# Kernel tuning notes

Measured on AMD Instinct MI355X. Metric: run time of the kernel, lower is better.

Reference implementation:

```python
import jax, jax.numpy as jnp
import numpy as np

N = 131072   # octree nodes at this depth
C = 192      # channels (depthwise)
K = 27       # 3x3x3 neighbor stencil
BN_EPS = 1e-5


def setup_inputs() -> dict:
    key = jax.random.key(0)
    k1, k2, k3 = jax.random.split(key, 3)
    data = jax.random.normal(k1, (N, C), dtype=jnp.float32)
    # Octree neighbor table: for each node, indices of its 27 stencil neighbors.
    neigh = jax.random.randint(k2, (N, K), 0, N)
    # Depthwise weights [K, C] (OctreeDWConv, use_bias=False)
    weight = jax.random.normal(k3, (K, C), dtype=jnp.float32) * 0.05
    gamma = jnp.ones((C,), dtype=jnp.float32)
    beta = jnp.zeros((C,), dtype=jnp.float32)
    return {"data": data, "neigh": neigh, "weight": weight,
            "gamma": gamma, "beta": beta}


def reference(data, neigh, weight, gamma, beta):
    # Depthwise octree conv: out[n, c] = sum_k data[neigh[n, k], c] * weight[k, c]
    # Scan over the 27 stencil taps so we never materialize the [N, K, C] gather.
    def step(acc, kin):
        idx_k, w_k = kin          # idx_k: [N], w_k: [C]
        return acc + data[idx_k] * w_k, None

    acc0 = jnp.zeros_like(data)
    out, _ = jax.lax.scan(step, acc0, (neigh.T, weight))  # out: [N, C]

    # BatchNorm1d (training mode: batch statistics over the node dimension)
    mean = jnp.mean(out, axis=0)
    var = jnp.var(out, axis=0)
    return (out - mean) * jax.lax.rsqrt(var + BN_EPS) * gamma + beta
```

## Files before the change

### kernel.cpp

```cpp
#include <hip/hip_runtime.h>


static constexpr int NN = 131072;
static constexpr int CC = 192;
static constexpr int KK = 27;
static constexpr int NB = 32;
static constexpr float BN_EPS = 1e-5f;

typedef float          f32x4 __attribute__((ext_vector_type(4)));
typedef unsigned short u16x4 __attribute__((ext_vector_type(4)));
typedef unsigned int   u32x4 __attribute__((ext_vector_type(4)));

__device__ __forceinline__ unsigned short f2bf_rne(float x) {
    unsigned u = __float_as_uint(x);
    return (unsigned short)((u + 0x7FFFu + ((u >> 16) & 1u)) >> 16);
}
__device__ __forceinline__ float bf2f(unsigned short b) {
    return __uint_as_float((unsigned)b << 16);
}

__global__ __launch_bounds__(256) void cvt_zero(
    const float* __restrict__ src, unsigned short* __restrict__ dst,
    float* __restrict__ stats )
{
    if (blockIdx.x < 2 && threadIdx.x < CC)
        stats[blockIdx.x * CC + threadIdx.x] = 0.f;

    const int tot    = NN * CC / 4;
    const int stride = gridDim.x * 256;
    for (int i = blockIdx.x * 256 + threadIdx.x; i < tot; i += stride) {
        const f32x4 v = __builtin_nontemporal_load(
            reinterpret_cast<const f32x4*>(src) + i);
        u16x4 o;
        o.x = f2bf_rne(v.x); o.y = f2bf_rne(v.y);
        o.z = f2bf_rne(v.z); o.w = f2bf_rne(v.w);
        reinterpret_cast<u16x4*>(dst)[i] = o;
    }
}

__global__ __launch_bounds__(192, 6) void conv_r8(
    const unsigned short* __restrict__ data_bf,
    const int*   __restrict__ neigh,
    const float* __restrict__ weight,
    unsigned short* __restrict__ conv_bf,
    float*       __restrict__ ch_sum,
    float*       __restrict__ ch_sumsq)
{
    const int c    = threadIdx.x;
    const int base = blockIdx.x * NB;

    float w[KK];
#pragma unroll
    for (int k = 0; k < KK; ++k) w[k] = weight[k * CC + c];

    float s = 0.f, ss = 0.f;

    for (int n = 0; n < NB; ++n) {
        const int node = base + n;
        const int* nrow = neigh + (size_t)node * KK;

        unsigned short r[KK];
#pragma unroll
        for (int k = 0; k < KK; ++k)
            r[k] = data_bf[(size_t)nrow[k] * CC + c];

        float acc = 0.f;
#pragma unroll
        for (int k = 0; k < KK; ++k)
            acc = fmaf(bf2f(r[k]), w[k], acc);

        __builtin_nontemporal_store(f2bf_rne(acc),
                                    &conv_bf[(size_t)node * CC + c]);
        s  += acc;
        ss += acc * acc;
    }

    atomicAdd(&ch_sum[c],   s);
    atomicAdd(&ch_sumsq[c], ss);
}

__global__ __launch_bounds__(192) void bn_apply_fused(
    const u32x4* __restrict__ conv_u4,
    const float* __restrict__ ch_sum,
    const float* __restrict__ ch_sumsq,
    const float* __restrict__ gamma,
    const float* __restrict__ beta,
    float* __restrict__ out)
{
    const int t  = threadIdx.x;
    const int cb = (t % 24) * 8;

    const float inv_n = 1.0f / (float)NN;
    float sc[8], bi[8];
#pragma unroll
    for (int j = 0; j < 8; ++j) {
        const float m = ch_sum[cb + j] * inv_n;
        const float v = ch_sumsq[cb + j] * inv_n - m * m;
        sc[j] = gamma[cb + j] * rsqrtf(v + BN_EPS);
        bi[j] = beta[cb + j] - m * sc[j];
    }

    f32x4* __restrict__ out4 = reinterpret_cast<f32x4*>(out);
    for (int nb = blockIdx.x; nb < NN / 8; nb += gridDim.x) {
        const int i8 = nb * 192 + t;
        const u32x4 u = __builtin_nontemporal_load(conv_u4 + i8);
        f32x4 a, b;
        a.x = fmaf(__uint_as_float(u.x << 16),         sc[0], bi[0]);
        a.y = fmaf(__uint_as_float(u.x & 0xFFFF0000u), sc[1], bi[1]);
        a.z = fmaf(__uint_as_float(u.y << 16),         sc[2], bi[2]);
        a.w = fmaf(__uint_as_float(u.y & 0xFFFF0000u), sc[3], bi[3]);
        b.x = fmaf(__uint_as_float(u.z << 16),         sc[4], bi[4]);
        b.y = fmaf(__uint_as_float(u.z & 0xFFFF0000u), sc[5], bi[5]);
        b.z = fmaf(__uint_as_float(u.w << 16),         sc[6], bi[6]);
        b.w = fmaf(__uint_as_float(u.w & 0xFFFF0000u), sc[7], bi[7]);
        __builtin_nontemporal_store(a, out4 + 2 * i8);
        __builtin_nontemporal_store(b, out4 + 2 * i8 + 1);
    }
}

__global__ __launch_bounds__(CC) void conv_bn_partial_f32(
    const float* __restrict__ data,
    const int*   __restrict__ neigh,
    const float* __restrict__ weight,
    float*       __restrict__ conv_out,
    float*       __restrict__ ch_sum,
    float*       __restrict__ ch_sumsq)
{
    const int c = threadIdx.x;
    const int base = blockIdx.x * NB;
    float w[KK];
#pragma unroll
    for (int k = 0; k < KK; ++k) w[k] = weight[k * CC + c];
    float s = 0.f, ss = 0.f;
    for (int n = 0; n < NB; ++n) {
        const int node = base + n;
        const int* nrow = neigh + node * KK;
        float acc = 0.f;
#pragma unroll
        for (int k = 0; k < KK; ++k)
            acc = fmaf(data[nrow[k] * CC + c], w[k], acc);
        conv_out[node * CC + c] = acc;
        s += acc; ss += acc * acc;
    }
    atomicAdd(&ch_sum[c], s);
    atomicAdd(&ch_sumsq[c], ss);
}

__global__ __launch_bounds__(192) void bn_apply_f32_fused(
    float* __restrict__ out,
    const float* __restrict__ ch_sum,
    const float* __restrict__ ch_sumsq,
    const float* __restrict__ gamma,
    const float* __restrict__ beta)
{
    const int t = threadIdx.x;
    const int g = t / 48;
    const int q = t - g * 48;
    const int cb = q * 4;
    const float inv_n = 1.0f / (float)NN;
    float4 sc, bi;
    float m0 = ch_sum[cb+0]*inv_n, m1 = ch_sum[cb+1]*inv_n;
    float m2 = ch_sum[cb+2]*inv_n, m3 = ch_sum[cb+3]*inv_n;
    sc.x = gamma[cb+0]*rsqrtf(ch_sumsq[cb+0]*inv_n - m0*m0 + BN_EPS);
    sc.y = gamma[cb+1]*rsqrtf(ch_sumsq[cb+1]*inv_n - m1*m1 + BN_EPS);
    sc.z = gamma[cb+2]*rsqrtf(ch_sumsq[cb+2]*inv_n - m2*m2 + BN_EPS);
    sc.w = gamma[cb+3]*rsqrtf(ch_sumsq[cb+3]*inv_n - m3*m3 + BN_EPS);
    bi.x = beta[cb+0] - m0*sc.x; bi.y = beta[cb+1] - m1*sc.y;
    bi.z = beta[cb+2] - m2*sc.z; bi.w = beta[cb+3] - m3*sc.w;
    for (int nb = blockIdx.x; nb < NN / 4; nb += gridDim.x) {
        const int i = (nb * 4 + g) * 48 + q;
        float4 v = reinterpret_cast<float4*>(out)[i];
        v.x = fmaf(v.x, sc.x, bi.x); v.y = fmaf(v.y, sc.y, bi.y);
        v.z = fmaf(v.z, sc.z, bi.z); v.w = fmaf(v.w, sc.w, bi.w);
        reinterpret_cast<float4*>(out)[i] = v;
    }
}

extern "C" void kernel_launch(void* const* d_in, const int* in_sizes, int n_in,
                              void* d_out, int out_size, void* d_ws, size_t ws_size,
                              hipStream_t stream) {
    const float* data   = (const float*)d_in[0];
    const int*   neigh  = (const int*)  d_in[1];
    const float* weight = (const float*)d_in[2];
    const float* gamma  = (const float*)d_in[3];
    const float* beta   = (const float*)d_in[4];
    float* out = (float*)d_out;

    float* stats    = (float*)d_ws;
    float* ch_sum   = stats;
    float* ch_sumsq = stats + CC;
    unsigned short* data_bf = (unsigned short*)((char*)d_ws + 4096);
    const size_t stage_bytes = (size_t)NN * CC * sizeof(unsigned short);
    unsigned short* conv_bf =
        (unsigned short*)((char*)d_ws + 4096 + stage_bytes);

    const size_t need_full = 4096 + 2 * stage_bytes;

    if (ws_size >= need_full) {
        cvt_zero<<<4096, 256, 0, stream>>>(data, data_bf, stats);
        conv_r8<<<NN / NB, 192, 0, stream>>>(
            data_bf, neigh, weight, conv_bf, ch_sum, ch_sumsq);
        bn_apply_fused<<<4096, 192, 0, stream>>>(
            (const u32x4*)conv_bf, ch_sum, ch_sumsq, gamma, beta, out);
    } else {
        hipMemsetAsync(stats, 0, 2 * CC * sizeof(float), stream);
        conv_bn_partial_f32<<<NN / NB, CC, 0, stream>>>(
            data, neigh, weight, out, ch_sum, ch_sumsq);
        bn_apply_f32_fused<<<8192, 192, 0, stream>>>(
            out, ch_sum, ch_sumsq, gamma, beta);
    }
}
```

Measured before the change: 412.6 us.

## Fuse convert, conv, and BN into one cooperative persistent kernel with grid syncs

Replaces the three kernel launches with a single cooperative kernel of 2048 blocks. It converts the input to bf16, runs the gather convolution over two node tiles per block, writes per-block partial statistics into the output buffer, reduces them, and applies BN, with grid.sync between phases. This removes launch gaps and per-block atomics on the stats but adds grid-wide barriers and caps residency at the cooperative grid size. Nontemporal loads and stores are also dropped in the fallback kernels. The old launches remain as a fallback if the cooperative launch fails.

```diff
diff --git a/kernel.cpp b/kernel.cpp
--- a/kernel.cpp
+++ b/kernel.cpp
@@ -1,10 +1,15 @@
 #include <hip/hip_runtime.h>
-
-
-static constexpr int NN = 131072;
-static constexpr int CC = 192;
-static constexpr int KK = 27;
-static constexpr int NB = 32;
+#include <hip/hip_cooperative_groups.h>
+
+namespace cg = cooperative_groups;
+
+
+static constexpr int NN   = 131072;
+static constexpr int CC   = 192;
+static constexpr int KK   = 27;
+static constexpr int NB   = 32;
+static constexpr int GRID = 2048;
+static constexpr int TPB  = 192;
 static constexpr float BN_EPS = 1e-5f;
 
 typedef float          f32x4 __attribute__((ext_vector_type(4)));
@@ -19,18 +24,127 @@
     return __uint_as_float((unsigned)b << 16);
 }
 
+__global__ __launch_bounds__(TPB, 6) void fused_all(
+    const float* __restrict__ data,
+    const int*   __restrict__ neigh,
+    const float* __restrict__ weight,
+    const float* __restrict__ gamma,
+    const float* __restrict__ beta,
+    float*       __restrict__ out,
+    unsigned short* __restrict__ data_bf,
+    unsigned short* __restrict__ conv_bf,
+    float*       __restrict__ stats)
+{
+    cg::grid_group grid = cg::this_grid();
+    const int t   = threadIdx.x;
+    const int bid = blockIdx.x;
+    float* partials = out;
+
+    if (bid < 2) stats[bid * TPB + t] = 0.f;
+    {
+        const int tot    = NN * CC / 4;
+        const int stride = GRID * TPB;
+        for (int i = bid * TPB + t; i < tot; i += stride) {
+            const f32x4 v = reinterpret_cast<const f32x4*>(data)[i];
+            u16x4 o;
+            o.x = f2bf_rne(v.x); o.y = f2bf_rne(v.y);
+            o.z = f2bf_rne(v.z); o.w = f2bf_rne(v.w);
+            reinterpret_cast<u16x4*>(data_bf)[i] = o;
+        }
+    }
+    __threadfence();
+    grid.sync();
+
+    {
+        float w[KK];
+#pragma unroll
+        for (int k = 0; k < KK; ++k) w[k] = weight[k * CC + t];
+
+        float s = 0.f, ss = 0.f;
+#pragma unroll 1
+        for (int gidx = 0; gidx < 2; ++gidx) {
+            const int base = (bid + gidx * GRID) * NB;
+            for (int n = 0; n < NB; ++n) {
+                const int node = base + n;
+                const int* nrow = neigh + (size_t)node * KK;
+
+                unsigned short r[KK];
+#pragma unroll
+                for (int k = 0; k < KK; ++k)
+                    r[k] = data_bf[(size_t)nrow[k] * CC + t];
+
+                float acc = 0.f;
+#pragma unroll
+                for (int k = 0; k < KK; ++k)
+                    acc = fmaf(bf2f(r[k]), w[k], acc);
+
+                conv_bf[(size_t)node * CC + t] = f2bf_rne(acc);
+                s  += acc;
+                ss += acc * acc;
+            }
+        }
+        partials[bid * 384 + t]       = s;
+        partials[bid * 384 + 192 + t] = ss;
+    }
+    __threadfence();
+    grid.sync();
+
+    if (bid < 16) {
+        float a0 = 0.f, a1 = 0.f;
+        const int r0 = bid * (GRID / 16);
+        for (int r = r0; r < r0 + GRID / 16; ++r) {
+            a0 += partials[r * 384 + t];
+            a1 += partials[r * 384 + 192 + t];
+        }
+        atomicAdd(&stats[t],       a0);
+        atomicAdd(&stats[192 + t], a1);
+    }
+    __threadfence();
+    grid.sync();
+
+    {
+        const int cb = (t % 24) * 8;
+        const float inv_n = 1.0f / (float)NN;
+        float sc[8], bi[8];
+#pragma unroll
+        for (int j = 0; j < 8; ++j) {
+            const float m = stats[cb + j] * inv_n;
+            const float v = stats[192 + cb + j] * inv_n - m * m;
+            sc[j] = gamma[cb + j] * rsqrtf(v + BN_EPS);
+            bi[j] = beta[cb + j] - m * sc[j];
+        }
+
+        const u32x4* __restrict__ conv_u4 =
+            reinterpret_cast<const u32x4*>(conv_bf);
+        f32x4* __restrict__ out4 = reinterpret_cast<f32x4*>(out);
+        for (int nb = bid; nb < NN / 8; nb += GRID) {
+            const int i8 = nb * TPB + t;
+            const u32x4 u = conv_u4[i8];
+            f32x4 a, b;
+            a.x = fmaf(__uint_as_float(u.x << 16),         sc[0], bi[0]);
+            a.y = fmaf(__uint_as_float(u.x & 0xFFFF0000u), sc[1], bi[1]);
+            a.z = fmaf(__uint_as_float(u.y << 16),         sc[2], bi[2]);
+            a.w = fmaf(__uint_as_float(u.y & 0xFFFF0000u), sc[3], bi[3]);
+            b.x = fmaf(__uint_as_float(u.z << 16),         sc[4], bi[4]);
+            b.y = fmaf(__uint_as_float(u.z & 0xFFFF0000u), sc[5], bi[5]);
+            b.z = fmaf(__uint_as_float(u.w << 16),         sc[6], bi[6]);
+            b.w = fmaf(__uint_as_float(u.w & 0xFFFF0000u), sc[7], bi[7]);
+            out4[2 * i8]     = a;
+            out4[2 * i8 + 1] = b;
+        }
+    }
+}
+
 __global__ __launch_bounds__(256) void cvt_zero(
     const float* __restrict__ src, unsigned short* __restrict__ dst,
-    float* __restrict__ stats )
+    float* __restrict__ stats)
 {
     if (blockIdx.x < 2 && threadIdx.x < CC)
         stats[blockIdx.x * CC + threadIdx.x] = 0.f;
-
     const int tot    = NN * CC / 4;
     const int stride = gridDim.x * 256;
     for (int i = blockIdx.x * 256 + threadIdx.x; i < tot; i += stride) {
-        const f32x4 v = __builtin_nontemporal_load(
-            reinterpret_cast<const f32x4*>(src) + i);
+        const f32x4 v = reinterpret_cast<const f32x4*>(src)[i];
         u16x4 o;
         o.x = f2bf_rne(v.x); o.y = f2bf_rne(v.y);
         o.z = f2bf_rne(v.z); o.w = f2bf_rne(v.w);
@@ -48,33 +162,25 @@
 {
     const int c    = threadIdx.x;
     const int base = blockIdx.x * NB;
-
     float w[KK];
 #pragma unroll
     for (int k = 0; k < KK; ++k) w[k] = weight[k * CC + c];
-
     float s = 0.f, ss = 0.f;
-
     for (int n = 0; n < NB; ++n) {
         const int node = base + n;
         const int* nrow = neigh + (size_t)node * KK;
-
         unsigned short r[KK];
 #pragma unroll
         for (int k = 0; k < KK; ++k)
             r[k] = data_bf[(size_t)nrow[k] * CC + c];
-
         float acc = 0.f;
 #pragma unroll
         for (int k = 0; k < KK; ++k)
             acc = fmaf(bf2f(r[k]), w[k], acc);
-
-        __builtin_nontemporal_store(f2bf_rne(acc),
-                                    &conv_bf[(size_t)node * CC + c]);
+        conv_bf[(size_t)node * CC + c] = f2bf_rne(acc);
         s  += acc;
         ss += acc * acc;
     }
-
     atomicAdd(&ch_sum[c],   s);
     atomicAdd(&ch_sumsq[c], ss);
 }
@@ -89,7 +195,6 @@
 {
     const int t  = threadIdx.x;
     const int cb = (t % 24) * 8;
-
     const float inv_n = 1.0f / (float)NN;
     float sc[8], bi[8];
 #pragma unroll
@@ -99,11 +204,10 @@
         sc[j] = gamma[cb + j] * rsqrtf(v + BN_EPS);
         bi[j] = beta[cb + j] - m * sc[j];
     }
-
     f32x4* __restrict__ out4 = reinterpret_cast<f32x4*>(out);
     for (int nb = blockIdx.x; nb < NN / 8; nb += gridDim.x) {
         const int i8 = nb * 192 + t;
-        const u32x4 u = __builtin_nontemporal_load(conv_u4 + i8);
+        const u32x4 u = conv_u4[i8];
         f32x4 a, b;
         a.x = fmaf(__uint_as_float(u.x << 16),         sc[0], bi[0]);
         a.y = fmaf(__uint_as_float(u.x & 0xFFFF0000u), sc[1], bi[1]);
@@ -113,8 +217,8 @@
         b.y = fmaf(__uint_as_float(u.z & 0xFFFF0000u), sc[5], bi[5]);
         b.z = fmaf(__uint_as_float(u.w << 16),         sc[6], bi[6]);
         b.w = fmaf(__uint_as_float(u.w & 0xFFFF0000u), sc[7], bi[7]);
-        __builtin_nontemporal_store(a, out4 + 2 * i8);
-        __builtin_nontemporal_store(b, out4 + 2 * i8 + 1);
+        out4[2 * i8]     = a;
+        out4[2 * i8 + 1] = b;
     }
 }
 
@@ -197,11 +301,19 @@
     const size_t need_full = 4096 + 2 * stage_bytes;
 
     if (ws_size >= need_full) {
-        cvt_zero<<<4096, 256, 0, stream>>>(data, data_bf, stats);
-        conv_r8<<<NN / NB, 192, 0, stream>>>(
-            data_bf, neigh, weight, conv_bf, ch_sum, ch_sumsq);
-        bn_apply_fused<<<4096, 192, 0, stream>>>(
-            (const u32x4*)conv_bf, ch_sum, ch_sumsq, gamma, beta, out);
+        void* args[] = {
+            (void*)&data, (void*)&neigh, (void*)&weight, (void*)&gamma,
+            (void*)&beta, (void*)&out, (void*)&data_bf, (void*)&conv_bf,
+            (void*)&stats };
+        hipError_t err = hipLaunchCooperativeKernel(
+            (const void*)fused_all, dim3(GRID), dim3(TPB), args, 0, stream);
+        if (err != hipSuccess) {
+            cvt_zero<<<4096, 256, 0, stream>>>(data, data_bf, stats);
+            conv_r8<<<NN / NB, 192, 0, stream>>>(
+                data_bf, neigh, weight, conv_bf, ch_sum, ch_sumsq);
+            bn_apply_fused<<<4096, 192, 0, stream>>>(
+                (const u32x4*)conv_bf, ch_sum, ch_sumsq, gamma, beta, out);
+        }
     } else {
         hipMemsetAsync(stats, 0, 2 * CC * sizeof(float), stream);
         conv_bn_partial_f32<<<NN / NB, CC, 0, stream>>>(
```

After: 1.339 ms. 3.25x slower.
